# Kernel tuning notes

Hardware: AMD Instinct MI355X
Metric: run time of the kernel (lower is better)

## Reference

```python
import jax, jax.numpy as jnp
import numpy as np

V, E, H, L, B = 50000, 300, 128, 32, 8


def setup_inputs() -> dict:
    key = jax.random.key(0)
    ks = jax.random.split(key, 12)
    s = 0.05
    d = {}
    d["premise"] = jax.random.randint(ks[0], (B, L), 0, V)
    d["hypothesis"] = jax.random.randint(ks[1], (B, L), 0, V)
    d["emb"] = jax.random.normal(ks[2], (V, E), jnp.float32) * s
    d["W_ih"] = jax.random.normal(ks[3], (8 * H, 2 * E), jnp.float32) * s
    d["b_ih"] = jnp.zeros((8 * H,), jnp.float32)
    d["W_hh"] = jax.random.normal(ks[4], (8 * H, 2 * H), jnp.float32) * s
    d["b_hh"] = jnp.zeros((8 * H,), jnp.float32)
    d["W_ch"] = jax.random.normal(ks[5], (H, 2 * H), jnp.float32) * s
    d["b_ch"] = jnp.zeros((H,), jnp.float32)
    d["W_cc"] = jax.random.normal(ks[6], (H, 2 * H), jnp.float32) * s
    d["b_cc"] = jnp.zeros((H,), jnp.float32)
    d["W1"] = jax.random.normal(ks[7], (H, H), jnp.float32) * s
    d["b1"] = jnp.zeros((H,), jnp.float32)
    d["W2"] = jax.random.normal(ks[8], (H, H), jnp.float32) * s
    d["b2"] = jnp.zeros((H,), jnp.float32)
    d["W3"] = jax.random.normal(ks[9], (3, H), jnp.float32) * s
    d["b3"] = jnp.zeros((3,), jnp.float32)
    return d


def _lstm_cell(x, h, c, W_ih, b_ih, W_hh, b_hh):
    # PyTorch LSTMCell gate order: i, f, g, o
    g = x @ W_ih.T + b_ih + h @ W_hh.T + b_hh
    i, f, gg, o = jnp.split(g, 4, axis=-1)
    c_new = jax.nn.sigmoid(f) * c + jax.nn.sigmoid(i) * jnp.tanh(gg)
    h_new = jax.nn.sigmoid(o) * jnp.tanh(c_new)
    return h_new, c_new


def reference(premise, hypothesis, emb, W_ih, b_ih, W_hh, b_hh,
              W_ch, b_ch, W_cc, b_cc, W1, b1, W2, b2, W3, b3):
    p = emb[premise]      # [B, L, E]
    hyp = emb[hypothesis]  # [B, L, E]
    Bn, Ln, En = p.shape
    Hn = W_ch.shape[0]
    p_t = jnp.swapaxes(p, 0, 1)    # [L, B, E]
    hyp_t = jnp.swapaxes(hyp, 0, 1)
    z = jnp.zeros((Bn, Hn), p.dtype)

    def row_step(row_carry, p_i):
        h_up, c_up = row_carry  # [L, B, H] from previous row (left deps)

        def col_step(carry, xs):
            h_low, c_low = carry       # [B, H] from previous column (lower deps)
            h_u, c_u, x_hyp = xs       # [B,H], [B,H], [B,E]
            x = jnp.concatenate([p_i, x_hyp], axis=-1)       # [B, 2E]
            h_in = jnp.concatenate([h_u, h_low], axis=-1)    # left then lower -> [B, 2H]
            c_in = jnp.concatenate([c_u, c_low], axis=-1)
            h_o, c_o = _lstm_cell(x, h_in, c_in, W_ih, b_ih, W_hh, b_hh)
            h_n = h_o @ W_ch.T + b_ch  # condense back to [B, H]
            c_n = c_o @ W_cc.T + b_cc
            return (h_n, c_n), (h_n, c_n)

        _, (h_row, c_row) = jax.lax.scan(col_step, (z, z), (h_up, c_up, hyp_t))
        return (h_row, c_row), None

    init = (jnp.zeros((Ln, Bn, Hn), p.dtype), jnp.zeros((Ln, Bn, Hn), p.dtype))
    (h_grid, _), _ = jax.lax.scan(row_step, init, p_t)
    h = h_grid[-1]  # h[L, L] corner state, [B, H]
    h = jax.nn.relu(h @ W1.T + b1)
    h = jax.nn.relu(h @ W2.T + b2)
    return jax.nn.softmax(h @ W3.T + b3, axis=1)
```

## Files before the change

kernel.cpp:

```cpp
#include <hip/hip_runtime.h>
#include <math.h>


typedef _Float16 h2 __attribute__((ext_vector_type(2)));
typedef unsigned long long ull;

__device__ __forceinline__ h2 pk_f16(float a, float b) {
    return __builtin_bit_cast(h2, __builtin_amdgcn_cvt_pkrtz(a, b));
}

#define HYP_OFF   0
#define WP_OFF    262144
#define B_OFF     524288
#define INITF_OFF 526336
#define WF_OFF    527360
#define HOT_OFF   531456
#define COT_OFF   793600
#define HOF_OFF   1317888

#define BASE 0xAAAAAAAAu

__device__ __forceinline__ float sigm(float x) { return 1.f / (1.f + __expf(-x)); }
__device__ __forceinline__ float tanh_fast(float x) { return 1.f - 2.f / (__expf(2.f * x) + 1.f); }

__device__ __forceinline__ unsigned ld_flag(const unsigned* p) {
    return __hip_atomic_load(p, __ATOMIC_RELAXED, __HIP_MEMORY_SCOPE_AGENT);
}
__device__ __forceinline__ void st_flag(unsigned* p, unsigned v) {
    __hip_atomic_store(p, v, __ATOMIC_RELAXED, __HIP_MEMORY_SCOPE_AGENT);
}
__device__ __forceinline__ float ld_f32(const float* p) {
    unsigned u = __hip_atomic_load((const unsigned*)p, __ATOMIC_RELAXED, __HIP_MEMORY_SCOPE_AGENT);
    return __uint_as_float(u);
}
__device__ __forceinline__ void st_f32(float* p, float v) {
    __hip_atomic_store((unsigned*)p, __float_as_uint(v), __ATOMIC_RELAXED, __HIP_MEMORY_SCOPE_AGENT);
}
__device__ __forceinline__ void st_u32(unsigned* p, unsigned v) {
    __hip_atomic_store(p, v, __ATOMIC_RELAXED, __HIP_MEMORY_SCOPE_AGENT);
}
__device__ __forceinline__ ull ld_u64(const ull* p) {
    return __hip_atomic_load(p, __ATOMIC_RELAXED, __HIP_MEMORY_SCOPE_AGENT);
}
__device__ __forceinline__ void st_u64(ull* p, ull v) {
    __hip_atomic_store(p, v, __ATOMIC_RELAXED, __HIP_MEMORY_SCOPE_AGENT);
}
__device__ __forceinline__ void wait_ge(const unsigned* f, unsigned target) {
    long spins = 0;
    while ((ld_flag(f) - BASE) < target) {
        __builtin_amdgcn_s_sleep(1);
        if (++spins > (1L << 22)) break;
    }
}
__device__ __forceinline__ void drain_vmem() {
    asm volatile("s_waitcnt vmcnt(0)" ::: "memory");
}

__global__ void __launch_bounds__(256, 1) grid_lstm_kernel(
    const int* __restrict__ premise, const int* __restrict__ hypothesis,
    const float* __restrict__ emb,
    const float* __restrict__ W_ih, const float* __restrict__ b_ih,
    const float* __restrict__ W_hh, const float* __restrict__ b_hh,
    const float* __restrict__ W_ch, const float* __restrict__ b_ch,
    const float* __restrict__ W_cc, const float* __restrict__ b_cc,
    const float* __restrict__ W1, const float* __restrict__ b1,
    const float* __restrict__ W2, const float* __restrict__ b2,
    const float* __restrict__ W3, const float* __restrict__ b3,
    float* __restrict__ out, float* __restrict__ ws)
{
    __shared__ h2    hAB[2048];
    __shared__ float sCo[2048];
    __shared__ float ppL[1024];
    __shared__ float red[8448];
    __shared__ float red2[2304];

    const int tid = threadIdx.x;
    const int bid = blockIdx.x;
    const int i   = bid & 31;
    const int c   = bid >> 5;

    float*    Hypproj = ws + HYP_OFF;
    unsigned* WP      = (unsigned*)(ws + WP_OFF);
    float*    BU      = ws + B_OFF;
    float*    BL      = ws + B_OFF + 1024;
    unsigned* InitF   = (unsigned*)(ws + INITF_OFF);
    unsigned* WF      = (unsigned*)(ws + WF_OFF);
    ull*      HoT     = (ull*)(ws + HOT_OFF);
    ull*      CoT     = (ull*)(ws + COT_OFF);
    ull*      HoF     = (ull*)(ws + HOF_OFF);

    const int tq = tid & 31, ks = tid >> 5;
    const int tl = tid & 31, bb = tid >> 5;

    {
        float* embs = red;
        for (int idx = tid; idx < 4800; idx += 256) {
            int side = idx / 2400, rem = idx - side * 2400;
            int b = rem / 300, e = rem - b * 300;
            const int* toks = side ? hypothesis : premise;
            embs[idx] = emb[(long)toks[b * 32 + i] * 300 + e];
        }
        __syncthreads();
        #pragma unroll 1
        for (int q = 0; q < 4; q++) {
            const int oo = tid + q * 256;
            const int b = oo >> 7, g = oo & 127;
            const int gr = (g >> 5) * 256 + c * 32 + (g & 31);
            float accP = b_ih[gr] + b_hh[gr];
            float accH = 0.f;
            const float* wp = W_ih + (long)gr * 600;
            const float* eP = embs + b * 300;
            const float* eH = embs + 2400 + b * 300;
            for (int e = 0; e < 300; e += 4) {
                float4 w1 = *(const float4*)(wp + e);
                float4 w2v = *(const float4*)(wp + 300 + e);
                float4 p4 = *(const float4*)(eP + e);
                float4 h4 = *(const float4*)(eH + e);
                accP += w1.x * p4.x + w1.y * p4.y + w1.z * p4.z + w1.w * p4.w;
                accH += w2v.x * h4.x + w2v.y * h4.y + w2v.z * h4.z + w2v.w * h4.w;
            }
            st_f32(&Hypproj[i * 8192 + b * 1024 + gr], accH);
            ppL[b * 128 + g] = accP;
        }
        __syncthreads();
    }

    {
        const int tr = tid >> 6, col = (tid & 63) * 4;
        const int r  = bid * 4 + tr;
        float u[4] = {0.f, 0.f, 0.f, 0.f}, l[4] = {0.f, 0.f, 0.f, 0.f};
        const float* whU = W_hh + (long)r * 256;
        const float* whL = whU + 128;
        for (int k = 0; k < 128; k++) {
            const float wu = whU[k], wl = whL[k];
            float4 wc = *(const float4*)(W_ch + (long)k * 256 + col);
            u[0] += wu * wc.x; u[1] += wu * wc.y; u[2] += wu * wc.z; u[3] += wu * wc.w;
            l[0] += wl * wc.x; l[1] += wl * wc.y; l[2] += wl * wc.z; l[3] += wl * wc.w;
        }
        unsigned* wrow = WP + (long)r * 256;
        st_u32(&wrow[col / 2],       __builtin_bit_cast(unsigned, __builtin_amdgcn_cvt_pkrtz(u[0], u[1])));
        st_u32(&wrow[col / 2 + 1],   __builtin_bit_cast(unsigned, __builtin_amdgcn_cvt_pkrtz(u[2], u[3])));
        st_u32(&wrow[128 + col / 2],     __builtin_bit_cast(unsigned, __builtin_amdgcn_cvt_pkrtz(l[0], l[1])));
        st_u32(&wrow[128 + col / 2 + 1], __builtin_bit_cast(unsigned, __builtin_amdgcn_cvt_pkrtz(l[2], l[3])));
        if ((tid & 63) == 0) {
            float su = 0.f, sl = 0.f;
            for (int k = 0; k < 128; k++) { su += whU[k] * b_ch[k]; sl += whL[k] * b_ch[k]; }
            st_f32(&BU[r], su); st_f32(&BL[r], sl);
        }
    }
    drain_vmem();
    __syncthreads();
    if (tid == 0) st_flag(&InitF[bid * 4], BASE + 1u);

    wait_ge(&InitF[tid * 4], 1u);
    __syncthreads();

    h2 w[4][32];
    #pragma unroll
    for (int a = 0; a < 4; a++) {
        const unsigned* src = WP + (long)(a * 256 + c * 32 + tq) * 256 + ks * 32;
        #pragma unroll
        for (int m = 0; m < 16; m++) {
            ull u2 = ld_u64((const ull*)(src + m * 2));
            w[a][2 * m]     = __builtin_bit_cast(h2, (unsigned)u2);
            w[a][2 * m + 1] = __builtin_bit_cast(h2, (unsigned)(u2 >> 32));
        }
    }
    float4 w3[8];
    {
        const float* wr = W_cc + (long)((c & 3) * 32 + tq) * 256 + ks * 32;
        #pragma unroll
        for (int m = 0; m < 8; m++) w3[m] = *(const float4*)(wr + m * 4);
    }
    float bUv[4], bLv[4];
    #pragma unroll
    for (int a = 0; a < 4; a++) {
        bUv[a] = ld_f32(&BU[a * 256 + c * 32 + tl]);
        bLv[a] = ld_f32(&BL[a * 256 + c * 32 + tl]);
    }

    #pragma unroll 1
    for (int j = 0; j < 32; j++) {
        const bool upok = (i > 0), lfok = (j > 0);
        const bool cok  = (c < 4) ? upok : lfok;
        const int  jl   = lfok ? (j - 1) : 0;

        const unsigned upTag = (unsigned)((i - 1) * 32 + j + 1);
        const unsigned lfTag = (unsigned)(i * 32 + j);
        const unsigned coTag = (c < 4) ? upTag : lfTag;

        {
            const unsigned* fp = nullptr;
            unsigned tgt = 0;
            if (upok && tid < 32) {
                fp = &WF[(((i - 1) * 8 + (tid >> 2)) * 4 + (tid & 3)) * 4];
                tgt = (unsigned)(j + 1);
            } else if (lfok && tid >= 32 && tid < 60) {
                int s = tid - 32;
                int cc = s >> 2;
                cc += (cc >= c) ? 1 : 0;
                fp = &WF[((i * 8 + cc) * 4 + (s & 3)) * 4];
                tgt = (unsigned)j;
            }
            if (fp) wait_ge(fp, tgt);
        }
        __syncthreads();

        const ull* HoUpT = HoT + (size_t)(((i - 1) & 3) * 32 + j) * 1024;
        const ull* HoLfT = HoT + (size_t)((i & 3) * 32 + jl) * 1024;
        const ull* CoST  = (c < 4)
            ? CoT + (size_t)(((i - 1) & 3) * 32 + j) * 2048
            : CoT + (size_t)((i & 3) * 32 + jl) * 2048;
        const int hi = tid >> 7, kk = tid & 127;

        float hyv[4];
        #pragma unroll
        for (int a = 0; a < 4; a++)
            hyv[a] = ld_f32(&Hypproj[j * 8192 + bb * 1024 + a * 256 + c * 32 + tl]);

        ull uv[4] = {0, 0, 0, 0}, lv[4] = {0, 0, 0, 0};
        ull cv[8] = {0, 0, 0, 0, 0, 0, 0, 0};
        unsigned pend = (upok ? 0x000Fu : 0u) | (lfok ? 0x00F0u : 0u) | (cok ? 0xFF00u : 0u);
        long spins = 0;
        while (pend) {
            #pragma unroll
            for (int r = 0; r < 4; r++) {
                if (pend & (1u << r))        uv[r] = ld_u64(HoUpT + (2 * r + hi) * 128 + kk);
                if (pend & (0x10u << r))     lv[r] = ld_u64(HoLfT + (2 * r + hi) * 128 + kk);
                if (pend & (0x100u << 2*r))  cv[2*r]   = ld_u64(CoST + (2 * r + hi) * 256 + 2 * kk);
                if (pend & (0x200u << 2*r))  cv[2*r+1] = ld_u64(CoST + (2 * r + hi) * 256 + 2 * kk + 1);
            }
            #pragma unroll
            for (int r = 0; r < 4; r++) {
                if ((pend & (1u << r))       && (unsigned)(uv[r] >> 32) == upTag)      pend &= ~(1u << r);
                if ((pend & (0x10u << r))    && (unsigned)(lv[r] >> 32) == lfTag)      pend &= ~(0x10u << r);
                if ((pend & (0x100u << 2*r)) && (unsigned)(cv[2*r] >> 32) == coTag)    pend &= ~(0x100u << 2*r);
                if ((pend & (0x200u << 2*r)) && (unsigned)(cv[2*r+1] >> 32) == coTag)  pend &= ~(0x200u << 2*r);
            }
            if (pend) {
                __builtin_amdgcn_s_sleep(1);
                if (++spins > (1L << 22)) break;
            }
        }
        __builtin_amdgcn_sched_barrier(0);
        #pragma unroll
        for (int r = 0; r < 4; r++) {
            const int b = 2 * r + hi;
            hAB[b * 256 + kk]       = __builtin_bit_cast(h2, (unsigned)uv[r]);
            hAB[b * 256 + 128 + kk] = __builtin_bit_cast(h2, (unsigned)lv[r]);
            sCo[b * 256 + 2 * kk]     = __uint_as_float((unsigned)cv[2*r]);
            sCo[b * 256 + 2 * kk + 1] = __uint_as_float((unsigned)cv[2*r+1]);
        }
        __syncthreads();

        float acc[4][8], a3[8];
        #pragma unroll
        for (int a = 0; a < 4; a++)
            #pragma unroll
            for (int b = 0; b < 8; b++) acc[a][b] = 0.f;
        #pragma unroll
        for (int b = 0; b < 8; b++) a3[b] = 0.f;
        #pragma unroll
        for (int b = 0; b < 8; b++) {
            const h2*    hb = hAB + b * 256 + ks * 32;
            const float* cb = sCo + b * 256 + ks * 32;
            #pragma unroll
            for (int m4 = 0; m4 < 8; m4++) {
                uint4 hu = *(const uint4*)(hb + m4 * 4);
                h2 h0 = __builtin_bit_cast(h2, hu.x);
                h2 h1 = __builtin_bit_cast(h2, hu.y);
                h2 h2v = __builtin_bit_cast(h2, hu.z);
                h2 h3 = __builtin_bit_cast(h2, hu.w);
                #pragma unroll
                for (int a = 0; a < 4; a++) {
                    acc[a][b] = __builtin_amdgcn_fdot2(w[a][m4 * 4],     h0,  acc[a][b], false);
                    acc[a][b] = __builtin_amdgcn_fdot2(w[a][m4 * 4 + 1], h1,  acc[a][b], false);
                    acc[a][b] = __builtin_amdgcn_fdot2(w[a][m4 * 4 + 2], h2v, acc[a][b], false);
                    acc[a][b] = __builtin_amdgcn_fdot2(w[a][m4 * 4 + 3], h3,  acc[a][b], false);
                }
                float4 cv4 = *(const float4*)(cb + m4 * 4);
                a3[b] += w3[m4].x * cv4.x + w3[m4].y * cv4.y + w3[m4].z * cv4.z + w3[m4].w * cv4.w;
            }
        }
        #pragma unroll
        for (int a = 0; a < 4; a++)
            #pragma unroll
            for (int b = 0; b < 8; b++) red[tid * 33 + a * 8 + b] = acc[a][b];
        #pragma unroll
        for (int b = 0; b < 8; b++) red2[tid * 9 + b] = a3[b];
        __syncthreads();

        {
            float g4[4];
            #pragma unroll
            for (int a = 0; a < 4; a++) {
                float s = 0.f;
                #pragma unroll
                for (int k = 0; k < 8; k++)
                    s += red[(k * 32 + tl) * 33 + a * 8 + bb];
                s += ppL[bb * 128 + a * 32 + tl] + hyv[a];
                if (upok) s += bUv[a];
                if (lfok) s += bLv[a];
                g4[a] = s;
            }
            float ci = 0.f;
            #pragma unroll
            for (int k = 0; k < 8; k++) ci += red2[(k * 32 + tl) * 9 + bb];
            if (cok) ci += b_cc[(c & 3) * 32 + tl];
            const float cnew = sigm(g4[1]) * ci + sigm(g4[0]) * tanh_fast(g4[2]);
            const float hnew = sigm(g4[3]) * tanh_fast(cnew);

            const unsigned myTag = (unsigned)(i * 32 + j + 1);
            const ull tagHi = ((ull)myTag) << 32;
            const int slot = (i & 3) * 32 + j;

            st_u64(&CoT[(size_t)slot * 2048 + bb * 256 + c * 32 + tl],
                   tagHi | (ull)__float_as_uint(cnew));
            const float hOdd = __shfl_xor(hnew, 1);
            if ((tl & 1) == 0)
                st_u64(&HoT[(size_t)slot * 1024 + bb * 128 + c * 16 + (tl >> 1)],
                       tagHi | (ull)__builtin_bit_cast(unsigned, pk_f16(hnew, hOdd)));
            if (i == 31 && j == 31)
                st_u64(&HoF[bb * 256 + c * 32 + tl],
                       tagHi | (ull)__float_as_uint(hnew));
        }
        if ((tid & 63) == 0)
            st_flag(&WF[((i * 8 + c) * 4 + (tid >> 6)) * 4], BASE + (unsigned)(j + 1));
    }

    if (bid == 31) {
        if (tid < 32)
            wait_ge(&WF[((31 * 8 + (tid >> 2)) * 4 + (tid & 3)) * 4], 32u);
        __syncthreads();
        const unsigned fTag = 1024u;
        float hov[8] = {0.f, 0.f, 0.f, 0.f, 0.f, 0.f, 0.f, 0.f};
        unsigned pf = 0xFFu;
        long spins = 0;
        while (pf) {
            ull tv[8];
            #pragma unroll
            for (int r = 0; r < 8; r++)
                if (pf & (1u << r)) tv[r] = ld_u64(HoF + r * 256 + tid);
            #pragma unroll
            for (int r = 0; r < 8; r++)
                if ((pf & (1u << r)) && (unsigned)(tv[r] >> 32) == fTag) {
                    hov[r] = __uint_as_float((unsigned)tv[r]);
                    pf &= ~(1u << r);
                }
            if (pf) {
                __builtin_amdgcn_s_sleep(1);
                if (++spins > (1L << 22)) break;
            }
        }
        #pragma unroll
        for (int r = 0; r < 8; r++) sCo[r * 256 + tid] = hov[r];
        __syncthreads();
        #pragma unroll 1
        for (int q = 0; q < 4; q++) {
            const int oo = tid + q * 256;
            const int b = oo >> 7, o = oo & 127;
            float a = b_ch[o];
            const float* wr = W_ch + (long)o * 256;
            const float* x = sCo + b * 256;
            for (int k = 0; k < 256; k += 4) {
                float4 wv = *(const float4*)(wr + k);
                float4 xv = *(const float4*)(x + k);
                a += wv.x * xv.x + wv.y * xv.y + wv.z * xv.z + wv.w * xv.w;
            }
            ppL[b * 128 + o] = a;
        }
        __syncthreads();
        float* m1 = red;
        float* m2 = red + 1024;
        for (int idx = tid; idx < 1024; idx += 256) {
            int b = idx >> 7, o = idx & 127;
            float a = b1[o];
            const float* wr = W1 + o * 128; const float* x = ppL + b * 128;
            for (int k = 0; k < 128; k++) a += wr[k] * x[k];
            m1[idx] = fmaxf(a, 0.f);
        }
        __syncthreads();
        for (int idx = tid; idx < 1024; idx += 256) {
            int b = idx >> 7, o = idx & 127;
            float a = b2[o];
            const float* wr = W2 + o * 128; const float* x = m1 + b * 128;
            for (int k = 0; k < 128; k++) a += wr[k] * x[k];
            m2[idx] = fmaxf(a, 0.f);
        }
        __syncthreads();
        if (tid < 8) {
            const int b = tid;
            float lg[3];
            for (int cc = 0; cc < 3; cc++) {
                float a = b3[cc];
                const float* wr = W3 + cc * 128; const float* x = m2 + b * 128;
                for (int k = 0; k < 128; k++) a += wr[k] * x[k];
                lg[cc] = a;
            }
            float m = fmaxf(lg[0], fmaxf(lg[1], lg[2]));
            float e0 = expf(lg[0] - m), e1 = expf(lg[1] - m), e2 = expf(lg[2] - m);
            float s = e0 + e1 + e2;
            out[b * 3 + 0] = e0 / s;
            out[b * 3 + 1] = e1 / s;
            out[b * 3 + 2] = e2 / s;
        }
    }
}

extern "C" void kernel_launch(void* const* d_in, const int* in_sizes, int n_in,
                              void* d_out, int out_size, void* d_ws, size_t ws_size,
                              hipStream_t stream) {
    const int*   premise    = (const int*)d_in[0];
    const int*   hypothesis = (const int*)d_in[1];
    const float* emb        = (const float*)d_in[2];
    const float* W_ih       = (const float*)d_in[3];
    const float* b_ih       = (const float*)d_in[4];
    const float* W_hh       = (const float*)d_in[5];
    const float* b_hh       = (const float*)d_in[6];
    const float* W_ch       = (const float*)d_in[7];
    const float* b_ch       = (const float*)d_in[8];
    const float* W_cc       = (const float*)d_in[9];
    const float* b_cc       = (const float*)d_in[10];
    const float* W1         = (const float*)d_in[11];
    const float* b1         = (const float*)d_in[12];
    const float* W2         = (const float*)d_in[13];
    const float* b2         = (const float*)d_in[14];
    const float* W3         = (const float*)d_in[15];
    const float* b3         = (const float*)d_in[16];
    float* out = (float*)d_out;
    float* ws  = (float*)d_ws;

    (void)in_sizes; (void)n_in; (void)out_size; (void)ws_size;

    grid_lstm_kernel<<<dim3(256), dim3(256), 0, stream>>>(
        premise, hypothesis, emb, W_ih, b_ih, W_hh, b_hh,
        W_ch, b_ch, W_cc, b_cc, W1, b1, W2, b2, W3, b3, out, ws);
}
```

Before: 659.6 us.

## Reduce K-split partial sums with lane shuffles and use one flag per block

Threads are remapped so each output row's 8-way K-split sits in adjacent lanes of one wave. Gate and cell partial sums are then reduced with xor shuffles instead of going through the LDS red/red2 arrays, which removes a __syncthreads and LDS traffic from every recurrence step. Progress flags shrink from four per block (one per wave) to a single flag written by thread 0, so fewer flags need to be polled. The Hypproj loads are issued before the dependency wait to hide their latency. Because only thread 0 now signals, the flag can be set before other waves have stored their outputs; correctness then depends on consumers still checking the tags carried with the data.

```diff
diff --git a/kernel.cpp b/kernel.cpp
--- a/kernel.cpp
+++ b/kernel.cpp
@@ -71,8 +71,7 @@
     __shared__ h2    hAB[2048];
     __shared__ float sCo[2048];
     __shared__ float ppL[1024];
-    __shared__ float red[8448];
-    __shared__ float red2[2304];
+    __shared__ float scr[4800];
 
     const int tid = threadIdx.x;
     const int bid = blockIdx.x;
@@ -89,11 +88,10 @@
     ull*      CoT     = (ull*)(ws + COT_OFF);
     ull*      HoF     = (ull*)(ws + HOF_OFF);
 
-    const int tq = tid & 31, ks = tid >> 5;
-    const int tl = tid & 31, bb = tid >> 5;
+    const int ksg = tid & 7, tqg = tid >> 3;
 
     {
-        float* embs = red;
+        float* embs = scr;
         for (int idx = tid; idx < 4800; idx += 256) {
             int side = idx / 2400, rem = idx - side * 2400;
             int b = rem / 300, e = rem - b * 300;
@@ -158,7 +156,7 @@
     h2 w[4][32];
     #pragma unroll
     for (int a = 0; a < 4; a++) {
-        const unsigned* src = WP + (long)(a * 256 + c * 32 + tq) * 256 + ks * 32;
+        const unsigned* src = WP + (long)(a * 256 + c * 32 + tqg) * 256 + ksg * 32;
         #pragma unroll
         for (int m = 0; m < 16; m++) {
             ull u2 = ld_u64((const ull*)(src + m * 2));
@@ -168,15 +166,15 @@
     }
     float4 w3[8];
     {
-        const float* wr = W_cc + (long)((c & 3) * 32 + tq) * 256 + ks * 32;
+        const float* wr = W_cc + (long)((c & 3) * 32 + tqg) * 256 + ksg * 32;
         #pragma unroll
         for (int m = 0; m < 8; m++) w3[m] = *(const float4*)(wr + m * 4);
     }
     float bUv[4], bLv[4];
     #pragma unroll
     for (int a = 0; a < 4; a++) {
-        bUv[a] = ld_f32(&BU[a * 256 + c * 32 + tl]);
-        bLv[a] = ld_f32(&BL[a * 256 + c * 32 + tl]);
+        bUv[a] = ld_f32(&BU[a * 256 + c * 32 + tqg]);
+        bLv[a] = ld_f32(&BL[a * 256 + c * 32 + tqg]);
     }
 
     #pragma unroll 1
@@ -189,20 +187,17 @@
         const unsigned lfTag = (unsigned)(i * 32 + j);
         const unsigned coTag = (c < 4) ? upTag : lfTag;
 
-        {
-            const unsigned* fp = nullptr;
-            unsigned tgt = 0;
-            if (upok && tid < 32) {
-                fp = &WF[(((i - 1) * 8 + (tid >> 2)) * 4 + (tid & 3)) * 4];
-                tgt = (unsigned)(j + 1);
-            } else if (lfok && tid >= 32 && tid < 60) {
-                int s = tid - 32;
-                int cc = s >> 2;
-                cc += (cc >= c) ? 1 : 0;
-                fp = &WF[((i * 8 + cc) * 4 + (s & 3)) * 4];
-                tgt = (unsigned)j;
-            }
-            if (fp) wait_ge(fp, tgt);
+        float hyv[4];
+        #pragma unroll
+        for (int a = 0; a < 4; a++)
+            hyv[a] = ld_f32(&Hypproj[j * 8192 + ksg * 1024 + a * 256 + c * 32 + tqg]);
+
+        if (upok && tid < 8) {
+            wait_ge(&WF[(tid * 32 + (i - 1)) * 16], (unsigned)(j + 1));
+        } else if (lfok && tid >= 8 && tid < 15) {
+            int s = tid - 8;
+            int cc = s + ((s >= c) ? 1 : 0);
+            wait_ge(&WF[(cc * 32 + i) * 16], (unsigned)j);
         }
         __syncthreads();
 
@@ -213,11 +208,6 @@
             : CoT + (size_t)((i & 3) * 32 + jl) * 2048;
         const int hi = tid >> 7, kk = tid & 127;
 
-        float hyv[4];
-        #pragma unroll
-        for (int a = 0; a < 4; a++)
-            hyv[a] = ld_f32(&Hypproj[j * 8192 + bb * 1024 + a * 256 + c * 32 + tl]);
-
         ull uv[4] = {0, 0, 0, 0}, lv[4] = {0, 0, 0, 0};
         ull cv[8] = {0, 0, 0, 0, 0, 0, 0, 0};
         unsigned pend = (upok ? 0x000Fu : 0u) | (lfok ? 0x00F0u : 0u) | (cok ? 0xFF00u : 0u);
@@ -262,8 +252,8 @@
         for (int b = 0; b < 8; b++) a3[b] = 0.f;
         #pragma unroll
         for (int b = 0; b < 8; b++) {
-            const h2*    hb = hAB + b * 256 + ks * 32;
-            const float* cb = sCo + b * 256 + ks * 32;
+            const h2*    hb = hAB + b * 256 + ksg * 32;
+            const float* cb = sCo + b * 256 + ksg * 32;
             #pragma unroll
             for (int m4 = 0; m4 < 8; m4++) {
                 uint4 hu = *(const uint4*)(hb + m4 * 4);
@@ -282,31 +272,37 @@
                 a3[b] += w3[m4].x * cv4.x + w3[m4].y * cv4.y + w3[m4].z * cv4.z + w3[m4].w * cv4.w;
             }
         }
+
         #pragma unroll
         for (int a = 0; a < 4; a++)
             #pragma unroll
-            for (int b = 0; b < 8; b++) red[tid * 33 + a * 8 + b] = acc[a][b];
-        #pragma unroll
-        for (int b = 0; b < 8; b++) red2[tid * 9 + b] = a3[b];
-        __syncthreads();
+            for (int b = 0; b < 8; b++) {
+                float v = acc[a][b];
+                v += __shfl_xor(v, 1);
+                v += __shfl_xor(v, 2);
+                v += __shfl_xor(v, 4);
+                acc[a][b] = v;
+            }
+        #pragma unroll
+        for (int b = 0; b < 8; b++) {
+            float v = a3[b];
+            v += __shfl_xor(v, 1);
+            v += __shfl_xor(v, 2);
+            v += __shfl_xor(v, 4);
+            a3[b] = v;
+        }
 
         {
             float g4[4];
             #pragma unroll
             for (int a = 0; a < 4; a++) {
-                float s = 0.f;
-                #pragma unroll
-                for (int k = 0; k < 8; k++)
-                    s += red[(k * 32 + tl) * 33 + a * 8 + bb];
-                s += ppL[bb * 128 + a * 32 + tl] + hyv[a];
+                float s = acc[a][ksg] + ppL[ksg * 128 + a * 32 + tqg] + hyv[a];
                 if (upok) s += bUv[a];
                 if (lfok) s += bLv[a];
                 g4[a] = s;
             }
-            float ci = 0.f;
-            #pragma unroll
-            for (int k = 0; k < 8; k++) ci += red2[(k * 32 + tl) * 9 + bb];
-            if (cok) ci += b_cc[(c & 3) * 32 + tl];
+            float ci = a3[ksg];
+            if (cok) ci += b_cc[(c & 3) * 32 + tqg];
             const float cnew = sigm(g4[1]) * ci + sigm(g4[0]) * tanh_fast(g4[2]);
             const float hnew = sigm(g4[3]) * tanh_fast(cnew);
 
@@ -314,23 +310,21 @@
             const ull tagHi = ((ull)myTag) << 32;
             const int slot = (i & 3) * 32 + j;
 
-            st_u64(&CoT[(size_t)slot * 2048 + bb * 256 + c * 32 + tl],
+            st_u64(&CoT[(size_t)slot * 2048 + ksg * 256 + c * 32 + tqg],
                    tagHi | (ull)__float_as_uint(cnew));
-            const float hOdd = __shfl_xor(hnew, 1);
-            if ((tl & 1) == 0)
-                st_u64(&HoT[(size_t)slot * 1024 + bb * 128 + c * 16 + (tl >> 1)],
+            const float hOdd = __shfl_xor(hnew, 8);
+            if ((tqg & 1) == 0)
+                st_u64(&HoT[(size_t)slot * 1024 + ksg * 128 + c * 16 + (tqg >> 1)],
                        tagHi | (ull)__builtin_bit_cast(unsigned, pk_f16(hnew, hOdd)));
             if (i == 31 && j == 31)
-                st_u64(&HoF[bb * 256 + c * 32 + tl],
+                st_u64(&HoF[ksg * 256 + c * 32 + tqg],
                        tagHi | (ull)__float_as_uint(hnew));
         }
-        if ((tid & 63) == 0)
-            st_flag(&WF[((i * 8 + c) * 4 + (tid >> 6)) * 4], BASE + (unsigned)(j + 1));
+        if (tid == 0) st_flag(&WF[bid * 16], BASE + (unsigned)(j + 1));
     }
 
     if (bid == 31) {
-        if (tid < 32)
-            wait_ge(&WF[((31 * 8 + (tid >> 2)) * 4 + (tid & 3)) * 4], 32u);
+        if (tid < 8) wait_ge(&WF[(tid * 32 + 31) * 16], 32u);
         __syncthreads();
         const unsigned fTag = 1024u;
         float hov[8] = {0.f, 0.f, 0.f, 0.f, 0.f, 0.f, 0.f, 0.f};
@@ -370,8 +364,8 @@
             ppL[b * 128 + o] = a;
         }
         __syncthreads();
-        float* m1 = red;
-        float* m2 = red + 1024;
+        float* m1 = scr;
+        float* m2 = scr + 1024;
         for (int idx = tid; idx < 1024; idx += 256) {
             int b = idx >> 7, o = idx & 127;
             float a = b1[o];
```

Result: slower. 885.3 us (+34.2%).
